# Kernel optimization log

Measured on AMD Instinct MI355X. Metric: run time of the kernel, lower is better.

Reference implementation:

```python
import jax, jax.numpy as jnp
import numpy as np

IN_C, OUT_C, K = 32, 32, 3
PAD = 1


def setup_inputs() -> dict:
    key = jax.random.key(0)
    kx, kw, kb = jax.random.split(key, 3)
    x = jax.random.normal(kx, (16, IN_C, 256, 256), dtype=jnp.float32)
    # Kaiming-ish init scale for the conv weight, matching nn.Conv2d defaults roughly
    fan_in = IN_C * K * K
    w = jax.random.normal(kw, (OUT_C, IN_C, K, K), dtype=jnp.float32) / np.sqrt(fan_in)
    b = jax.random.normal(kb, (OUT_C,), dtype=jnp.float32) * 0.01
    return {"x": x, "weight": w, "bias": b}


def reference(x, weight, bias):
    # Faithful math of SparseConv2d.forward: the block-sparse Triton path computes
    # the same result as a dense conv (zero blocks contribute zero), so the
    # reference is a standard 3x3 stride-1 pad-1 conv, NCHW / OIHW layout.
    y = jax.lax.conv_general_dilated(
        x, weight,
        window_strides=(1, 1),
        padding=((PAD, PAD), (PAD, PAD)),
        dimension_numbers=("NCHW", "OIHW", "NCHW"),
    )
    return y + bias[None, :, None, None]
```

## Files before the change

### kernel.cpp

```cpp
#include <hip/hip_runtime.h>


constexpr int N_  = 16;
constexpr int C_  = 32;
constexpr int OC_ = 32;
constexpr int H_  = 256;
constexpr int W_  = 256;

constexpr int WSTR = 40;
constexpr int RSTR = 258 * WSTR;

typedef __attribute__((ext_vector_type(8)))  short short8;
typedef __attribute__((ext_vector_type(16))) float float16;

static __device__ __forceinline__ unsigned short f2bf(float f) {
    unsigned int u = __float_as_uint(f);
    unsigned int r = (u + 0x7FFFu + ((u >> 16) & 1u)) >> 16;
    return (unsigned short)r;
}

__global__ __launch_bounds__(256, 2) void conv3x3_mfma_kernel(
    const float* __restrict__ x,
    const float* __restrict__ wgt,
    const float* __restrict__ bias,
    float* __restrict__ out)
{
    __shared__ __align__(16) unsigned short ldsX[3 * RSTR];
    __shared__ __align__(16) unsigned short ldsW[9 * 32 * 32];

    const int tid = threadIdx.x;

    const int id = blockIdx.x;
    const int L  = (id & 7) * 512 + (id >> 3);
    const int n  = L >> 8;
    const int h  = L & (H_ - 1);

    for (int i = tid; i < OC_ * C_ * 9; i += 256) {
        const float v = wgt[i];
        const int oc  = i / 288;
        const int rem = i - oc * 288;
        const int ic  = rem / 9;
        const int k9  = rem - ic * 9;
        ldsW[(k9 * 32 + oc) * 32 + ic] = f2bf(v);
    }

    const int wlo = tid & 15;
    const int ic2 = tid >> 4;
    #pragma unroll
    for (int r = 0; r < 3; ++r) {
        const int hy = h + r - 1;
        unsigned short* dst = &ldsX[r * RSTR];
        if (hy >= 0 && hy < H_) {
            const float* p0 = x + (((size_t)(n * C_ + 2 * ic2) * H_ + hy) * W_);
            const float* p1 = p0 + (size_t)H_ * W_;
            #pragma unroll
            for (int wb = 0; wb < 16; ++wb) {
                const int w = wb * 16 + wlo;
                const unsigned int u =
                    (unsigned int)f2bf(p0[w]) | ((unsigned int)f2bf(p1[w]) << 16);
                *(unsigned int*)&dst[(w + 1) * WSTR + 2 * ic2] = u;
            }
        } else {
            #pragma unroll
            for (int wb = 0; wb < 16; ++wb) {
                const int w = wb * 16 + wlo;
                *(unsigned int*)&dst[(w + 1) * WSTR + 2 * ic2] = 0u;
            }
        }
    }
    if (tid < 96) {
        const int r  = tid >> 5;
        const int q  = tid & 31;
        const int wi = (q & 16) ? 257 : 0;
        *(unsigned int*)&ldsX[r * RSTR + wi * WSTR + (q & 15) * 2] = 0u;
    }
    __syncthreads();

    const int lane = tid & 63;
    const int wv   = tid >> 6;
    const int col  = lane & 31;
    const int qd   = lane >> 5;

    float16 acc0, acc1;
    #pragma unroll
    for (int r = 0; r < 16; ++r) {
        const float bv = bias[(r & 3) + 8 * (r >> 2) + 4 * qd];
        acc0[r] = bv;
        acc1[r] = bv;
    }

    const int w0a = wv * 64;
    const int w0b = wv * 64 + 32;

    #pragma unroll
    for (int kh = 0; kh < 3; ++kh) {
        #pragma unroll
        for (int kw = 0; kw < 3; ++kw) {
            const int t9 = kh * 3 + kw;
            #pragma unroll
            for (int ih = 0; ih < 2; ++ih) {
                const short8 av =
                    *(const short8*)&ldsW[(t9 * 32 + col) * 32 + ih * 16 + qd * 8];
                const short8 b0 =
                    *(const short8*)&ldsX[kh * RSTR + (w0a + col + kw) * WSTR + ih * 16 + qd * 8];
                const short8 b1 =
                    *(const short8*)&ldsX[kh * RSTR + (w0b + col + kw) * WSTR + ih * 16 + qd * 8];
                acc0 = __builtin_amdgcn_mfma_f32_32x32x16_bf16(av, b0, acc0, 0, 0, 0);
                acc1 = __builtin_amdgcn_mfma_f32_32x32x16_bf16(av, b1, acc1, 0, 0, 0);
            }
        }
    }

    float* outp = out + (size_t)n * OC_ * H_ * W_ + (size_t)h * W_;
    #pragma unroll
    for (int r = 0; r < 16; ++r) {
        const int oc = (r & 3) + 8 * (r >> 2) + 4 * qd;
        outp[(size_t)oc * H_ * W_ + w0a + col] = acc0[r];
        outp[(size_t)oc * H_ * W_ + w0b + col] = acc1[r];
    }
}

extern "C" void kernel_launch(void* const* d_in, const int* in_sizes, int n_in,
                              void* d_out, int out_size, void* d_ws, size_t ws_size,
                              hipStream_t stream) {
    const float* x    = (const float*)d_in[0];
    const float* wgt  = (const float*)d_in[1];
    const float* bias = (const float*)d_in[2];
    float* out        = (float*)d_out;

    dim3 grid(N_ * H_);
    dim3 block(256);
    conv3x3_mfma_kernel<<<grid, block, 0, stream>>>(x, wgt, bias, out);
}
```

Baseline: 269.2 us.

## Stage input channels in two halves to shrink LDS and raise occupancy

Splits the 32 input channels into two 16-channel halves staged through a smaller LDS input buffer, with a barrier between halves, so LDS per block drops and launch bounds go from 2 to 3 blocks per SIMD group. Global loads become float2 vectors, and LDS strides change (20 for input, 36 for weights), with 8-element fragments read as two 4-element loads to keep alignment. The trade-off is an extra barrier and a serialized load-then-compute phase per half, plus possible register pressure at the higher occupancy target.

```diff
diff --git a/kernel.cpp b/kernel.cpp
--- a/kernel.cpp
+++ b/kernel.cpp
@@ -7,11 +7,13 @@
 constexpr int H_  = 256;
 constexpr int W_  = 256;
 
-constexpr int WSTR = 40;
-constexpr int RSTR = 258 * WSTR;
+constexpr int XSTR = 20;
+constexpr int XROW = 258 * XSTR;
+constexpr int WSTRD = 36;
 
-typedef __attribute__((ext_vector_type(8)))  short short8;
-typedef __attribute__((ext_vector_type(16))) float float16;
+typedef __attribute__((ext_vector_type(4)))  short short4v;
+typedef __attribute__((ext_vector_type(8)))  short short8v;
+typedef __attribute__((ext_vector_type(16))) float float16v;
 
 static __device__ __forceinline__ unsigned short f2bf(float f) {
     unsigned int u = __float_as_uint(f);
@@ -19,14 +21,24 @@
     return (unsigned short)r;
 }
 
-__global__ __launch_bounds__(256, 2) void conv3x3_mfma_kernel(
+static __device__ __forceinline__ unsigned pk2(float a, float b) {
+    return (unsigned)f2bf(a) | ((unsigned)f2bf(b) << 16);
+}
+
+static __device__ __forceinline__ short8v load8(const unsigned short* p) {
+    short4v lo = *(const short4v*)p;
+    short4v hi = *(const short4v*)(p + 4);
+    return __builtin_shufflevector(lo, hi, 0, 1, 2, 3, 4, 5, 6, 7);
+}
+
+__global__ __launch_bounds__(256, 3) void conv3x3_mfma_kernel(
     const float* __restrict__ x,
     const float* __restrict__ wgt,
     const float* __restrict__ bias,
     float* __restrict__ out)
 {
-    __shared__ __align__(16) unsigned short ldsX[3 * RSTR];
-    __shared__ __align__(16) unsigned short ldsW[9 * 32 * 32];
+    __shared__ __align__(16) unsigned short ldsX[3 * XROW];
+    __shared__ __align__(16) unsigned short ldsW[9 * 32 * WSTRD];
 
     const int tid = threadIdx.x;
 
@@ -40,48 +52,16 @@
         const int oc  = i / 288;
         const int rem = i - oc * 288;
         const int ic  = rem / 9;
-        const int k9  = rem - ic * 9;
-        ldsW[(k9 * 32 + oc) * 32 + ic] = f2bf(v);
+        const int t9  = rem - ic * 9;
+        ldsW[(t9 * 32 + oc) * WSTRD + ic] = f2bf(v);
     }
-
-    const int wlo = tid & 15;
-    const int ic2 = tid >> 4;
-    #pragma unroll
-    for (int r = 0; r < 3; ++r) {
-        const int hy = h + r - 1;
-        unsigned short* dst = &ldsX[r * RSTR];
-        if (hy >= 0 && hy < H_) {
-            const float* p0 = x + (((size_t)(n * C_ + 2 * ic2) * H_ + hy) * W_);
-            const float* p1 = p0 + (size_t)H_ * W_;
-            #pragma unroll
-            for (int wb = 0; wb < 16; ++wb) {
-                const int w = wb * 16 + wlo;
-                const unsigned int u =
-                    (unsigned int)f2bf(p0[w]) | ((unsigned int)f2bf(p1[w]) << 16);
-                *(unsigned int*)&dst[(w + 1) * WSTR + 2 * ic2] = u;
-            }
-        } else {
-            #pragma unroll
-            for (int wb = 0; wb < 16; ++wb) {
-                const int w = wb * 16 + wlo;
-                *(unsigned int*)&dst[(w + 1) * WSTR + 2 * ic2] = 0u;
-            }
-        }
-    }
-    if (tid < 96) {
-        const int r  = tid >> 5;
-        const int q  = tid & 31;
-        const int wi = (q & 16) ? 257 : 0;
-        *(unsigned int*)&ldsX[r * RSTR + wi * WSTR + (q & 15) * 2] = 0u;
-    }
-    __syncthreads();
 
     const int lane = tid & 63;
     const int wv   = tid >> 6;
     const int col  = lane & 31;
     const int qd   = lane >> 5;
 
-    float16 acc0, acc1;
+    float16v acc0, acc1;
     #pragma unroll
     for (int r = 0; r < 16; ++r) {
         const float bv = bias[(r & 3) + 8 * (r >> 2) + 4 * qd];
@@ -89,22 +69,59 @@
         acc1[r] = bv;
     }
 
+    const int wlo = tid & 31;
+    const int icp = tid >> 5;
     const int w0a = wv * 64;
     const int w0b = wv * 64 + 32;
 
-    #pragma unroll
-    for (int kh = 0; kh < 3; ++kh) {
+    for (int half = 0; half < 2; ++half) {
+        if (half) __syncthreads();
+
+        const int icg = half * 16 + 2 * icp;
         #pragma unroll
-        for (int kw = 0; kw < 3; ++kw) {
-            const int t9 = kh * 3 + kw;
+        for (int r = 0; r < 3; ++r) {
+            const int hy = h + r - 1;
+            unsigned short* dst = &ldsX[r * XROW];
+            if (hy >= 0 && hy < H_) {
+                const float* p0 = x + (((size_t)(n * C_ + icg) * H_ + hy) * W_);
+                const float* p1 = p0 + (size_t)H_ * W_;
+                #pragma unroll
+                for (int wb = 0; wb < 4; ++wb) {
+                    const int w = wb * 64 + 2 * wlo;
+                    const float2 a = *(const float2*)(p0 + w);
+                    const float2 b = *(const float2*)(p1 + w);
+                    *(unsigned*)&dst[(w + 1) * XSTR + 2 * icp] = pk2(a.x, b.x);
+                    *(unsigned*)&dst[(w + 2) * XSTR + 2 * icp] = pk2(a.y, b.y);
+                }
+            } else {
+                #pragma unroll
+                for (int wb = 0; wb < 4; ++wb) {
+                    const int w = wb * 64 + 2 * wlo;
+                    *(unsigned*)&dst[(w + 1) * XSTR + 2 * icp] = 0u;
+                    *(unsigned*)&dst[(w + 2) * XSTR + 2 * icp] = 0u;
+                }
+            }
+        }
+        if (tid < 24) {
+            const int r  = tid >> 3;
+            const int q  = tid & 7;
+            const int wi = (q & 4) ? 257 : 0;
+            const int c  = q & 3;
+            *(unsigned long long*)&ldsX[r * XROW + wi * XSTR + c * 4] = 0ull;
+        }
+        __syncthreads();
+
+        #pragma unroll
+        for (int kh = 0; kh < 3; ++kh) {
             #pragma unroll
-            for (int ih = 0; ih < 2; ++ih) {
-                const short8 av =
-                    *(const short8*)&ldsW[(t9 * 32 + col) * 32 + ih * 16 + qd * 8];
-                const short8 b0 =
-                    *(const short8*)&ldsX[kh * RSTR + (w0a + col + kw) * WSTR + ih * 16 + qd * 8];
-                const short8 b1 =
-                    *(const short8*)&ldsX[kh * RSTR + (w0b + col + kw) * WSTR + ih * 16 + qd * 8];
+            for (int kw = 0; kw < 3; ++kw) {
+                const int t9 = kh * 3 + kw;
+                const short8v av =
+                    load8(&ldsW[(t9 * 32 + col) * WSTRD + half * 16 + qd * 8]);
+                const short8v b0 =
+                    load8(&ldsX[kh * XROW + (w0a + col + kw) * XSTR + qd * 8]);
+                const short8v b1 =
+                    load8(&ldsX[kh * XROW + (w0b + col + kw) * XSTR + qd * 8]);
                 acc0 = __builtin_amdgcn_mfma_f32_32x32x16_bf16(av, b0, acc0, 0, 0, 0);
                 acc1 = __builtin_amdgcn_mfma_f32_32x32x16_bf16(av, b1, acc1, 0, 0, 0);
             }
```

After: 262.3 us. 1.03x faster.
